# Optimization experiments

Hardware: AMD Instinct MI355X
Metric: run time of the kernel (lower is better)

Reference implementation:

```python
import jax, jax.numpy as jnp
import numpy as np

HEADS, HEAD_DIM, NQP, NVP = 12, 16, 4, 8
NODE_DIM, EDGE_DIM = 384, 128
B, N = 1, 768


def setup_inputs() -> dict:
    key = jax.random.key(0)
    ks = jax.random.split(key, 12)
    node_features = jax.random.normal(ks[0], (B, N, NODE_DIM), dtype=jnp.float32)
    edge_features = jax.random.normal(ks[1], (B, N, N, EDGE_DIM), dtype=jnp.float32)
    # random valid rotations via QR of gaussian matrices (well-conditioned for inverse)
    A = jax.random.normal(ks[2], (B, N, 3, 3), dtype=jnp.float32)
    Q, _ = jnp.linalg.qr(A)
    R = Q
    t = jax.random.normal(ks[3], (B, N, 3), dtype=jnp.float32)
    def lin(k, din, dout):
        return jax.random.normal(k, (din, dout), dtype=jnp.float32) / np.sqrt(din)
    Wqkv = lin(ks[4], NODE_DIM, 3 * HEADS * HEAD_DIM)
    Wvqk = lin(ks[5], NODE_DIM, 2 * 3 * NQP * HEADS)
    Wvv = lin(ks[6], NODE_DIM, 3 * NVP * HEADS)
    Webias = lin(ks[7], EDGE_DIM, HEADS)
    fin_in = HEADS * EDGE_DIM + HEADS * HEAD_DIM + HEADS * NVP * 4
    Wfin = lin(ks[8], fin_in, NODE_DIM)
    bfin = jnp.zeros((NODE_DIM,), dtype=jnp.float32)
    return {"node_features": node_features, "edge_features": edge_features,
            "R": R, "t": t, "Wqkv": Wqkv, "Wvqk": Wvqk, "Wvv": Wvv,
            "Webias": Webias, "Wfin": Wfin, "bfin": bfin}


def _ipa(node_features, edge_features, R, t, Wqkv, Wvqk, Wvv, Webias, Wfin, bfin):
    b, n, _ = node_features.shape
    h, d, p, pv = HEADS, HEAD_DIM, NQP, NVP
    # scalar q, k, v: [b, h, n, d]
    qkv = (node_features @ Wqkv).reshape(b, n, 3, h, d)
    sq, sk, sv = [jnp.transpose(qkv[:, :, i], (0, 2, 1, 3)) for i in range(3)]
    node_scalar = jnp.einsum('bhid,bhjd->bhij', sq, sk) * (d ** -0.5)
    edge_bias = jnp.einsum('bijd,dh->bhij', edge_features, Webias)
    # vector q/k in local frames: [b, h, n, p, 3]
    vqk = (node_features @ Wvqk).reshape(b, n, 2, h, p, 3)
    vq = jnp.transpose(vqk[:, :, 0], (0, 2, 1, 3, 4))
    vk = jnp.transpose(vqk[:, :, 1], (0, 2, 1, 3, 4))
    t_e = t[:, None, :, None, :]  # [b,1,n,1,3]
    gq = jnp.einsum('bnij,bhnpj->bhnpi', R, vq) + t_e
    gk = jnp.einsum('bnij,bhnpj->bhnpi', R, vk) + t_e
    # ||gk_i - gq_j||^2 summed over (p,3), expanded to avoid [b,h,n,n,p,3]
    wc = np.sqrt(2.0 / 9.0 / p) / 2.0
    k_sq = jnp.sum(gk * gk, axis=(-1, -2))  # [b,h,n]
    q_sq = jnp.sum(gq * gq, axis=(-1, -2))  # [b,h,n]
    cross = jnp.einsum('bhipd,bhjpd->bhij', gk, gq)
    dist = (k_sq[:, :, :, None] + q_sq[:, :, None, :] - 2.0 * cross) * wc
    attn = jax.nn.softmax((node_scalar + edge_bias - dist) * (3 ** -0.5), axis=-1)
    # aggregations
    edge_out = jnp.einsum('bhij,bijd->bihd', attn, edge_features)     # [b,n,h,edge_dim]
    scalar_out = jnp.einsum('bhij,bhjd->bihd', attn, sv)              # [b,n,h,d]
    vv = (node_features @ Wvv).reshape(b, n, h, pv, 3)
    vv = jnp.transpose(vv, (0, 2, 1, 3, 4))                            # [b,h,n,pv,3]
    gvv = jnp.einsum('bnij,bhnpj->bhnpi', R, vv) + t_e
    att_v = jnp.einsum('bhij,bhjpd->bihpd', attn, gvv)                # [b,n,h,pv,3]
    Rinv = jnp.linalg.inv(R)
    local_v = jnp.einsum('bnij,bnhpj->bnhpi', Rinv, att_v - t[:, :, None, None, :])
    v_len = jnp.sqrt(jnp.sum(local_v * local_v, axis=-1))             # [b,n,h,pv]
    combined = jnp.concatenate([
        edge_out.reshape(b, n, -1),
        scalar_out.reshape(b, n, -1),
        local_v.reshape(b, n, -1),
        v_len.reshape(b, n, -1),
    ], axis=-1)
    return node_features + combined @ Wfin + bfin


def reference(node_features, edge_features, R, t, Wqkv, Wvqk, Wvv, Webias, Wfin, bfin):
    return _ipa(node_features, edge_features, R, t, Wqkv, Wvqk, Wvv, Webias, Wfin, bfin)
```

## Files before the change

kernel.cpp:

```cpp
#include <hip/hip_runtime.h>
#include <cmath>


namespace {

constexpr int NN = 768;
constexpr int NH = 12;

constexpr float S3 = 0.5773502691896258f;
constexpr float C1 = 0.25f * S3;
constexpr float C2 = 0.23570226039551584f * S3;
constexpr float C3 = 0.11785113019775792f * S3;

typedef float f32x4 __attribute__((ext_vector_type(4)));
typedef short bf16x8 __attribute__((ext_vector_type(8)));
typedef unsigned int u32x4 __attribute__((ext_vector_type(4)));
typedef unsigned int u32x2 __attribute__((ext_vector_type(2)));
typedef _Float16 f16x2 __attribute__((ext_vector_type(2)));

#define LGKM0 asm volatile("s_waitcnt lgkmcnt(0)" ::: "memory")
#define SCHED0 __builtin_amdgcn_sched_barrier(0)

__device__ inline unsigned cvt_pk_bf16(float lo, float hi) {
  unsigned r;
  asm volatile("v_cvt_pk_bf16_f32 %0, %1, %2" : "=v"(r) : "v"(lo), "v"(hi));
  return r;
}

__device__ inline float fdot2(unsigned a, unsigned b, float c) {
#if __has_builtin(__builtin_amdgcn_fdot2)
  return __builtin_amdgcn_fdot2(__builtin_bit_cast(f16x2, a),
                                __builtin_bit_cast(f16x2, b), c, false);
#else
  union U { unsigned u; _Float16 h[2]; } x, y;
  x.u = a; y.u = b;
  return c + (float)x.h[0] * (float)y.h[0] + (float)x.h[1] * (float)y.h[1];
#endif
}

__device__ inline u32x2 tr_read(unsigned addr) {
  u32x2 d;
  asm volatile("ds_read_b64_tr_b16 %0, %1" : "=v"(d) : "v"(addr));
  return d;
}

__device__ inline f32x4 mfma16(u32x2 a, u32x2 b, f32x4 c) {
  asm volatile("v_mfma_f32_16x16x16_bf16 %0, %1, %2, %0"
               : "+v"(c) : "v"(a), "v"(b));
  return c;
}

__device__ inline unsigned pkf16(float a, float b) {
  union U { _Float16 h[2]; unsigned u; } x;
  x.h[0] = (_Float16)a; x.h[1] = (_Float16)b;
  return x.u;
}

__global__ __launch_bounds__(288) void k_proj(const float* __restrict__ node,
    const float* __restrict__ Wqkv, const float* __restrict__ Wvqk,
    const float* __restrict__ Wvv, float* __restrict__ proj) {
  __shared__ __align__(16) float nl[4][384];
  const int i0 = blockIdx.x * 4;
  const int tid = threadIdx.x;
  for (int idx = tid; idx < 4 * 384; idx += 288)
    ((float*)nl)[idx] = node[(size_t)i0 * 384 + idx];
  __syncthreads();
  const int c0 = tid * 4;
  const float* W; int ld, col;
  if (c0 < 576)      { W = Wqkv; ld = 576; col = c0; }
  else if (c0 < 864) { W = Wvqk; ld = 288; col = c0 - 576; }
  else               { W = Wvv;  ld = 288; col = c0 - 864; }
  float4 acc[4];
#pragma unroll
  for (int r = 0; r < 4; ++r) acc[r] = make_float4(0.f, 0.f, 0.f, 0.f);
#pragma unroll 4
  for (int k = 0; k < 384; ++k) {
    const float4 w4 = *(const float4*)&W[(size_t)k * ld + col];
#pragma unroll
    for (int r = 0; r < 4; ++r) {
      const float nv = nl[r][k];
      acc[r].x += nv * w4.x; acc[r].y += nv * w4.y;
      acc[r].z += nv * w4.z; acc[r].w += nv * w4.w;
    }
  }
#pragma unroll
  for (int r = 0; r < 4; ++r)
    *(float4*)&proj[(size_t)(i0 + r) * 1152 + c0] = acc[r];
}

__global__ __launch_bounds__(256) void k_geom(const float* __restrict__ proj,
    const float* __restrict__ R, const float* __restrict__ t,
    unsigned* __restrict__ Bph, unsigned* __restrict__ Sgh,
    float* __restrict__ V) {
  const int gid = blockIdx.x * 256 + threadIdx.x;
  if (gid >= NN * NH) return;
  const int n = gid / NH, h = gid % NH;
  const float* pr = proj + (size_t)n * 1152;
  const float* Rn = R + n * 9;
  const float t0 = t[n * 3 + 0], t1 = t[n * 3 + 1], t2 = t[n * 3 + 2];
  const size_t hn = (size_t)h * NN + n;
  unsigned* bp = Bph + hn * 16;
  unsigned* sg = Sgh + ((size_t)n * NH + h) * 16;
#pragma unroll
  for (int m = 0; m < 8; ++m) {
    bp[m] = pkf16(C1 * pr[(12 + h) * 16 + 2 * m], C1 * pr[(12 + h) * 16 + 2 * m + 1]);
    sg[m] = pkf16(pr[h * 16 + 2 * m], pr[h * 16 + 2 * m + 1]);
    V[hn * 40 + 2 * m]     = pr[(24 + h) * 16 + 2 * m];
    V[hn * 40 + 2 * m + 1] = pr[(24 + h) * 16 + 2 * m + 1];
  }
  float gq[12], gk[12];
  float qs = 0.f, ks = 0.f;
#pragma unroll
  for (int p = 0; p < 4; ++p) {
    {
      const float vx = pr[576 + (h * 4 + p) * 3 + 0];
      const float vy = pr[576 + (h * 4 + p) * 3 + 1];
      const float vz = pr[576 + (h * 4 + p) * 3 + 2];
      const float g0 = Rn[0] * vx + Rn[1] * vy + Rn[2] * vz + t0;
      const float g1 = Rn[3] * vx + Rn[4] * vy + Rn[5] * vz + t1;
      const float g2 = Rn[6] * vx + Rn[7] * vy + Rn[8] * vz + t2;
      gq[p * 3 + 0] = g0; gq[p * 3 + 1] = g1; gq[p * 3 + 2] = g2;
      qs += g0 * g0 + g1 * g1 + g2 * g2;
    }
    {
      const float vx = pr[576 + ((12 + h) * 4 + p) * 3 + 0];
      const float vy = pr[576 + ((12 + h) * 4 + p) * 3 + 1];
      const float vz = pr[576 + ((12 + h) * 4 + p) * 3 + 2];
      const float g0 = Rn[0] * vx + Rn[1] * vy + Rn[2] * vz + t0;
      const float g1 = Rn[3] * vx + Rn[4] * vy + Rn[5] * vz + t1;
      const float g2 = Rn[6] * vx + Rn[7] * vy + Rn[8] * vz + t2;
      gk[p * 3 + 0] = g0; gk[p * 3 + 1] = g1; gk[p * 3 + 2] = g2;
      ks += g0 * g0 + g1 * g1 + g2 * g2;
    }
  }
#pragma unroll
  for (int m = 0; m < 6; ++m) {
    bp[8 + m] = pkf16(C2 * gq[2 * m], C2 * gq[2 * m + 1]);
    sg[8 + m] = pkf16(gk[2 * m], gk[2 * m + 1]);
  }
  bp[14] = pkf16(-C3 * qs, 1.0f);
  sg[14] = pkf16(1.0f, -C3 * ks);
  bp[15] = 0u; sg[15] = 0u;
#pragma unroll
  for (int p = 0; p < 8; ++p) {
    const float vx = pr[864 + (h * 8 + p) * 3 + 0];
    const float vy = pr[864 + (h * 8 + p) * 3 + 1];
    const float vz = pr[864 + (h * 8 + p) * 3 + 2];
    V[hn * 40 + 16 + p * 3 + 0] = Rn[0] * vx + Rn[1] * vy + Rn[2] * vz + t0;
    V[hn * 40 + 16 + p * 3 + 1] = Rn[3] * vx + Rn[4] * vy + Rn[5] * vz + t1;
    V[hn * 40 + 16 + p * 3 + 2] = Rn[6] * vx + Rn[7] * vy + Rn[8] * vz + t2;
  }
}

__global__ __launch_bounds__(256, 3) void k_fused(
    const float* __restrict__ edge, const float* __restrict__ Webias,
    const unsigned* __restrict__ Bph, const unsigned* __restrict__ Sgh,
    unsigned* __restrict__ pTu, float* __restrict__ m_t,
    float* __restrict__ eout, float* __restrict__ msm,
    float* __restrict__ linv) {
  __shared__ __align__(16) unsigned short etS[4][2112];
  __shared__ __align__(16) float Osh[4][8][16][16];
  __shared__ float msh[4][16];
  __shared__ float lsh[4][16];
  const int i = blockIdx.x;
  const int tid = threadIdx.x;
  const int lane = tid & 63;
  const int w = __builtin_amdgcn_readfirstlane(tid >> 6);
  const int g = lane >> 4;
  const int c16 = lane & 15;
  const int hc = c16 < 12 ? c16 : 11;

  const unsigned etbase =
      (unsigned)(uintptr_t)(__attribute__((address_space(3))) unsigned short*)&etS[w][0];

  bf16x8 wbfrag[4];
#pragma unroll
  for (int kk = 0; kk < 4; ++kk) {
    union Pk { unsigned u[4]; bf16x8 v; } pk;
#pragma unroll
    for (int e2 = 0; e2 < 4; ++e2) {
      const int d = kk * 32 + g * 8 + 2 * e2;
      const float lo = (c16 < 12) ? S3 * Webias[d * 12 + c16] : 0.f;
      const float hi = (c16 < 12) ? S3 * Webias[(d + 1) * 12 + c16] : 0.f;
      pk.u[e2] = cvt_pk_bf16(lo, hi);
    }
    wbfrag[kk] = pk.v;
  }

  const unsigned* sgp = Sgh + ((size_t)i * NH + hc) * 16;
  const u32x4 sg0 = *(const u32x4*)(sgp + 0);
  const u32x4 sg1 = *(const u32x4*)(sgp + 4);
  const u32x4 sg2 = *(const u32x4*)(sgp + 8);
  const u32x4 sg3 = *(const u32x4*)(sgp + 12);

  float m = -3.0e38f;
  float lsum = 0.f;
  f32x4 acc[8];
#pragma unroll
  for (int dt = 0; dt < 8; ++dt) acc[dt] = (f32x4){0.f, 0.f, 0.f, 0.f};

  float4 ra[8];
  auto load8 = [&](int t) {
    const int jw = t * 64 + w * 16;
#pragma unroll
    for (int q = 0; q < 4; ++q) {
      const int f8 = lane + 64 * q;
      const int j = f8 >> 4, c8 = f8 & 15;
      const float* gp = &edge[((size_t)(i * NN + jw + j)) * 128 + c8 * 8];
      ra[2 * q]     = *(const float4*)gp;
      ra[2 * q + 1] = *(const float4*)(gp + 4);
    }
  };
  auto store8 = [&]() {
#pragma unroll
    for (int q = 0; q < 4; ++q) {
      const int f8 = lane + 64 * q;
      const int j = f8 >> 4, c8 = f8 & 15;
      u32x4 pk;
      pk.x = cvt_pk_bf16(ra[2 * q].x,     ra[2 * q].y);
      pk.y = cvt_pk_bf16(ra[2 * q].z,     ra[2 * q].w);
      pk.z = cvt_pk_bf16(ra[2 * q + 1].x, ra[2 * q + 1].y);
      pk.w = cvt_pk_bf16(ra[2 * q + 1].z, ra[2 * q + 1].w);
      *(u32x4*)&etS[w][(c8 >> 1) * 264 + j * 16 + 8 * (c8 & 1)] = pk;
    }
  };

  load8(0);

#pragma unroll 1
  for (int t = 0; t < 12; ++t) {
    const int tw = t * 4 + w;
    LGKM0;
    store8();
    SCHED0;
    if (t < 11) load8(t + 1);

    f32x4 ebacc = {0.f, 0.f, 0.f, 0.f};
#pragma unroll
    for (int kk = 0; kk < 4; ++kk) {
      const int dt = 2 * kk + (g >> 1);
      const bf16x8 a = *(const bf16x8*)&etS[w][dt * 264 + c16 * 16 + 8 * (g & 1)];
      ebacc = __builtin_amdgcn_mfma_f32_16x16x32_bf16(a, wbfrag[kk], ebacc, 0, 0, 0);
    }

    float lg[4];
#pragma unroll
    for (int r = 0; r < 4; ++r) {
      const unsigned* bpp = Bph + ((size_t)hc * NN + (tw * 16 + 4 * g + r)) * 16;
      const u32x4 b0 = *(const u32x4*)(bpp + 0);
      const u32x4 b1 = *(const u32x4*)(bpp + 4);
      const u32x4 b2 = *(const u32x4*)(bpp + 8);
      const u32x4 b3 = *(const u32x4*)(bpp + 12);
      float a = ebacc[r];
      a = fdot2(b0.x, sg0.x, a); a = fdot2(b0.y, sg0.y, a);
      a = fdot2(b0.z, sg0.z, a); a = fdot2(b0.w, sg0.w, a);
      a = fdot2(b1.x, sg1.x, a); a = fdot2(b1.y, sg1.y, a);
      a = fdot2(b1.z, sg1.z, a); a = fdot2(b1.w, sg1.w, a);
      a = fdot2(b2.x, sg2.x, a); a = fdot2(b2.y, sg2.y, a);
      a = fdot2(b2.z, sg2.z, a); a = fdot2(b2.w, sg2.w, a);
      a = fdot2(b3.x, sg3.x, a); a = fdot2(b3.y, sg3.y, a);
      a = fdot2(b3.z, sg3.z, a);
      lg[r] = a;
    }

    const float lmax = fmaxf(fmaxf(lg[0], lg[1]), fmaxf(lg[2], lg[3]));
    if (__any(lmax > m + 6.f)) {
      float tm = lmax;
      tm = fmaxf(tm, __shfl_xor(tm, 16, 64));
      tm = fmaxf(tm, __shfl_xor(tm, 32, 64));
      const float mn = fmaxf(m, tm);
      const float f = __expf(m - mn);
      m = mn;
      lsum *= f;
      float fr[4];
#pragma unroll
      for (int r = 0; r < 4; ++r) fr[r] = __shfl(f, 4 * g + r, 64);
#pragma unroll
      for (int dt = 0; dt < 8; ++dt) {
        acc[dt][0] *= fr[0]; acc[dt][1] *= fr[1];
        acc[dt][2] *= fr[2]; acc[dt][3] *= fr[3];
      }
    }
    float p0 = __expf(lg[0] - m), p1 = __expf(lg[1] - m);
    float p2 = __expf(lg[2] - m), p3 = __expf(lg[3] - m);
    lsum += (p0 + p1) + (p2 + p3);
    const unsigned pk0 = cvt_pk_bf16(p0, p1);
    const unsigned pk1 = cvt_pk_bf16(p2, p3);
    pTu[((size_t)i * 48 + tw) * 128 + g * 16 + c16]      = pk0;
    pTu[((size_t)i * 48 + tw) * 128 + 64 + g * 16 + c16] = pk1;
    if (g == 0) m_t[((size_t)i * 48 + tw) * 16 + c16] = m;

    u32x2 bfr[8];
#pragma unroll
    for (int dt = 0; dt < 8; ++dt) {
      const unsigned addr = etbase + (unsigned)(dt * 528 + g * 128 + c16 * 8);
      bfr[dt] = tr_read(addr);
    }
    LGKM0; SCHED0;
    u32x2 apk; apk.x = pk0; apk.y = pk1;
#pragma unroll
    for (int dt = 0; dt < 8; ++dt) acc[dt] = mfma16(apk, bfr[dt], acc[dt]);
  }

#pragma unroll
  for (int dt = 0; dt < 8; ++dt)
#pragma unroll
    for (int r = 0; r < 4; ++r)
      Osh[w][dt][c16][4 * g + r] = acc[dt][r];
  float ls = lsum;
  ls += __shfl_xor(ls, 16, 64);
  ls += __shfl_xor(ls, 32, 64);
  if (lane < 16) { msh[w][lane] = m; lsh[w][lane] = ls; }
  __syncthreads();
  for (int idx = tid; idx < 12 * 128; idx += 256) {
    const int h = idx >> 7, d = idx & 127;
    const int dt = d >> 4, dp = d & 15;
    const float m0 = msh[0][h], m1 = msh[1][h], m2 = msh[2][h], m3 = msh[3][h];
    const float mb = fmaxf(fmaxf(m0, m1), fmaxf(m2, m3));
    const float f0 = __expf(m0 - mb), f1 = __expf(m1 - mb);
    const float f2 = __expf(m2 - mb), f3 = __expf(m3 - mb);
    const float lb = lsh[0][h] * f0 + lsh[1][h] * f1 + lsh[2][h] * f2 + lsh[3][h] * f3;
    const float O = Osh[0][dt][dp][h] * f0 + Osh[1][dt][dp][h] * f1
                  + Osh[2][dt][dp][h] * f2 + Osh[3][dt][dp][h] * f3;
    eout[(size_t)i * 1536 + h * 128 + d] = O / lb;
    if (d == 0) {
      msm[(size_t)h * NN + i] = mb;
      linv[(size_t)h * NN + i] = 1.0f / lb;
    }
  }
}

__global__ __launch_bounds__(320) void k_scav(const unsigned* __restrict__ pTu,
    const float* __restrict__ m_t, const float* __restrict__ msm,
    const float* __restrict__ linv, const float* __restrict__ V,
    float* __restrict__ scav) {
  __shared__ __align__(16) float At[64][20];
  __shared__ __align__(16) float Vt[64][40];
  __shared__ __align__(16) float red[320 * 8];
  const int i0 = blockIdx.x * 16;
  const int h  = blockIdx.y;
  const int tid = threadIdx.x;
  const int js = tid / 80, rem = tid % 80;
  const int rg = rem / 20, cp = rem % 20;
  float2 a0 = {0.f, 0.f}, a1 = {0.f, 0.f}, a2 = {0.f, 0.f}, a3 = {0.f, 0.f};
  for (int jt = 0; jt < 12; ++jt) {
    __syncthreads();
    for (int idx = tid; idx < 1024; idx += 320) {
      const int r = idx >> 6, jj = idx & 63;
      const int i = i0 + r;
      const int tw = jt * 4 + (jj >> 4);
      const int gg = (jj & 15) >> 2, e = jj & 3;
      const unsigned u = pTu[((size_t)i * 48 + tw) * 128 + (e >> 1) * 64 + gg * 16 + h];
      const float p = __uint_as_float((e & 1) ? (u & 0xffff0000u) : (u << 16));
      const float fac = __expf(m_t[((size_t)i * 48 + tw) * 16 + h] - msm[(size_t)h * NN + i])
                      * linv[(size_t)h * NN + i];
      At[jj][r] = p * fac;
    }
    for (int idx = tid; idx < 2560; idx += 320) {
      const int jj = idx / 40, c = idx % 40;
      Vt[jj][c] = V[((size_t)h * NN + jt * 64 + jj) * 40 + c];
    }
    __syncthreads();
#pragma unroll 4
    for (int s = 0; s < 16; ++s) {
      const int jj = js * 16 + s;
      const float4 a4 = *(const float4*)&At[jj][rg * 4];
      const float2 b2 = *(const float2*)&Vt[jj][cp * 2];
      a0.x += a4.x * b2.x; a0.y += a4.x * b2.y;
      a1.x += a4.y * b2.x; a1.y += a4.y * b2.y;
      a2.x += a4.z * b2.x; a2.y += a4.z * b2.y;
      a3.x += a4.w * b2.x; a3.y += a4.w * b2.y;
    }
  }
  __syncthreads();
  *(float4*)&red[tid * 8 + 0] = make_float4(a0.x, a0.y, a1.x, a1.y);
  *(float4*)&red[tid * 8 + 4] = make_float4(a2.x, a2.y, a3.x, a3.y);
  __syncthreads();
  if (tid < 80) {
    const int rg2 = tid / 20, cp2 = tid % 20;
    float4 s0 = make_float4(0.f, 0.f, 0.f, 0.f), s1 = s0;
#pragma unroll
    for (int q = 0; q < 4; ++q) {
      const float4 r0 = *(const float4*)&red[(tid + q * 80) * 8 + 0];
      const float4 r1 = *(const float4*)&red[(tid + q * 80) * 8 + 4];
      s0.x += r0.x; s0.y += r0.y; s0.z += r0.z; s0.w += r0.w;
      s1.x += r1.x; s1.y += r1.y; s1.z += r1.z; s1.w += r1.w;
    }
    const size_t base = (size_t)h * NN + i0 + rg2 * 4;
    *(float2*)&scav[(base + 0) * 40 + cp2 * 2] = make_float2(s0.x, s0.y);
    *(float2*)&scav[(base + 1) * 40 + cp2 * 2] = make_float2(s0.z, s0.w);
    *(float2*)&scav[(base + 2) * 40 + cp2 * 2] = make_float2(s1.x, s1.y);
    *(float2*)&scav[(base + 3) * 40 + cp2 * 2] = make_float2(s1.z, s1.w);
  }
}

__global__ __launch_bounds__(256) void k_comb(
    const float* __restrict__ R, const float* __restrict__ t,
    const float* __restrict__ eout, const float* __restrict__ scav,
    float* __restrict__ comb) {
  const int i0 = blockIdx.x * 4;
  const int tid = threadIdx.x;
  __shared__ float rinv[4][9];
  __shared__ float tl[4][3];
  if (tid < 4) {
    const int i = i0 + tid;
    const float* Rn = R + i * 9;
    const float r00 = Rn[0], r01 = Rn[1], r02 = Rn[2];
    const float r10 = Rn[3], r11 = Rn[4], r12 = Rn[5];
    const float r20 = Rn[6], r21 = Rn[7], r22 = Rn[8];
    const float det = r00 * (r11 * r22 - r12 * r21)
                    - r01 * (r10 * r22 - r12 * r20)
                    + r02 * (r10 * r21 - r11 * r20);
    const float id = 1.0f / det;
    rinv[tid][0] = (r11 * r22 - r12 * r21) * id;
    rinv[tid][1] = (r02 * r21 - r01 * r22) * id;
    rinv[tid][2] = (r01 * r12 - r02 * r11) * id;
    rinv[tid][3] = (r12 * r20 - r10 * r22) * id;
    rinv[tid][4] = (r00 * r22 - r02 * r20) * id;
    rinv[tid][5] = (r02 * r10 - r00 * r12) * id;
    rinv[tid][6] = (r10 * r21 - r11 * r20) * id;
    rinv[tid][7] = (r01 * r20 - r00 * r21) * id;
    rinv[tid][8] = (r00 * r11 - r01 * r10) * id;
    tl[tid][0] = t[i * 3 + 0]; tl[tid][1] = t[i * 3 + 1]; tl[tid][2] = t[i * 3 + 2];
  }
  __syncthreads();
  for (int idx = tid; idx < 4 * 2112; idx += 256) {
    const int r = idx / 2112, k = idx % 2112;
    const int i = i0 + r;
    float val;
    if (k < 1536) {
      val = eout[(size_t)i * 1536 + k];
    } else if (k < 1728) {
      const int s = k - 1536, h = s >> 4, d = s & 15;
      val = scav[((size_t)h * NN + i) * 40 + d];
    } else if (k < 2016) {
      const int s = k - 1728, h = s / 24, rem = s % 24, p = rem / 3, x = rem % 3;
      const float* av = scav + ((size_t)h * NN + i) * 40 + 16 + p * 3;
      const float a0 = av[0] - tl[r][0], a1 = av[1] - tl[r][1], a2 = av[2] - tl[r][2];
      val = rinv[r][x * 3 + 0] * a0 + rinv[r][x * 3 + 1] * a1 + rinv[r][x * 3 + 2] * a2;
    } else {
      const int s = k - 2016, h = s >> 3, p = s & 7;
      const float* av = scav + ((size_t)h * NN + i) * 40 + 16 + p * 3;
      const float a0 = av[0] - tl[r][0], a1 = av[1] - tl[r][1], a2 = av[2] - tl[r][2];
      const float l0 = rinv[r][0] * a0 + rinv[r][1] * a1 + rinv[r][2] * a2;
      const float l1 = rinv[r][3] * a0 + rinv[r][4] * a1 + rinv[r][5] * a2;
      const float l2 = rinv[r][6] * a0 + rinv[r][7] * a1 + rinv[r][8] * a2;
      val = sqrtf(l0 * l0 + l1 * l1 + l2 * l2);
    }
    comb[(size_t)i * 2112 + k] = val;
  }
}

__global__ __launch_bounds__(256) void k_finalA(
    const float* __restrict__ comb, const float* __restrict__ Wfin,
    float* __restrict__ partial) {
  __shared__ __align__(16) float cl[64][36];
  __shared__ __align__(16) float wl[32][68];
  const int i0 = blockIdx.x * 64;
  const int c0 = blockIdx.y * 64;
  const int k0 = blockIdx.z * 192;
  const int tid = threadIdx.x;
  const int cq = tid & 15, rq = tid >> 4;
  float4 acc[4];
#pragma unroll
  for (int r = 0; r < 4; ++r) acc[r] = make_float4(0.f, 0.f, 0.f, 0.f);
  for (int sub = 0; sub < 6; ++sub) {
    const int kc = k0 + sub * 32;
    __syncthreads();
#pragma unroll
    for (int half = 0; half < 2; ++half) {
      const int qi = tid + half * 256;
      const int r = qi >> 3, kq = qi & 7;
      *(float4*)&cl[r][kq * 4] = *(const float4*)&comb[(size_t)(i0 + r) * 2112 + kc + kq * 4];
      const int kk = qi >> 4, cc = qi & 15;
      *(float4*)&wl[kk][cc * 4] = *(const float4*)&Wfin[(size_t)(kc + kk) * 384 + c0 + cc * 4];
    }
    __syncthreads();
#pragma unroll
    for (int k4 = 0; k4 < 8; ++k4) {
      float4 a[4], wv[4];
#pragma unroll
      for (int r = 0; r < 4; ++r) a[r] = *(const float4*)&cl[rq * 4 + r][k4 * 4];
#pragma unroll
      for (int q = 0; q < 4; ++q) wv[q] = *(const float4*)&wl[k4 * 4 + q][cq * 4];
#pragma unroll
      for (int r = 0; r < 4; ++r) {
        acc[r].x += a[r].x * wv[0].x + a[r].y * wv[1].x + a[r].z * wv[2].x + a[r].w * wv[3].x;
        acc[r].y += a[r].x * wv[0].y + a[r].y * wv[1].y + a[r].z * wv[2].y + a[r].w * wv[3].y;
        acc[r].z += a[r].x * wv[0].z + a[r].y * wv[1].z + a[r].z * wv[2].z + a[r].w * wv[3].z;
        acc[r].w += a[r].x * wv[0].w + a[r].y * wv[1].w + a[r].z * wv[2].w + a[r].w * wv[3].w;
      }
    }
  }
#pragma unroll
  for (int r = 0; r < 4; ++r)
    *(float4*)&partial[((size_t)blockIdx.z * NN + i0 + rq * 4 + r) * 384 + c0 + cq * 4] = acc[r];
}

__global__ __launch_bounds__(256) void k_finalB(const float* __restrict__ node,
    const float* __restrict__ partial, const float* __restrict__ bfin,
    float* __restrict__ out) {
  const int gid = blockIdx.x * 256 + threadIdx.x;
  const int i = gid / 96, cq = gid % 96;
  float4 v = *(const float4*)&node[(size_t)i * 384 + cq * 4];
  const float4 b = *(const float4*)&bfin[cq * 4];
  v.x += b.x; v.y += b.y; v.z += b.z; v.w += b.w;
#pragma unroll
  for (int s = 0; s < 11; ++s) {
    const float4 p = *(const float4*)&partial[((size_t)s * NN + i) * 384 + cq * 4];
    v.x += p.x; v.y += p.y; v.z += p.z; v.w += p.w;
  }
  *(float4*)&out[(size_t)i * 384 + cq * 4] = v;
}

}

extern "C" void kernel_launch(void* const* d_in, const int* in_sizes, int n_in,
                              void* d_out, int out_size, void* d_ws, size_t ws_size,
                              hipStream_t stream) {
  const float* node   = (const float*)d_in[0];
  const float* edge   = (const float*)d_in[1];
  const float* R      = (const float*)d_in[2];
  const float* t      = (const float*)d_in[3];
  const float* Wqkv   = (const float*)d_in[4];
  const float* Wvqk   = (const float*)d_in[5];
  const float* Wvv    = (const float*)d_in[6];
  const float* Webias = (const float*)d_in[7];
  const float* Wfin   = (const float*)d_in[8];
  const float* bfin   = (const float*)d_in[9];
  float* out = (float*)d_out;

  float* ws = (float*)d_ws;
  float*    proj = ws;
  float*    V    = proj + 884736;
  unsigned* Bph  = (unsigned*)(V + 368640);
  unsigned* Sgh  = Bph + 147456;
  unsigned* pTu  = Sgh + 147456;
  float*    m_t  = (float*)(pTu + 4718592);
  float*    eout = m_t + 589824;
  float*    scav = eout + 1179648;
  float*    msm  = scav + 368640;
  float*    linv = msm + 9216;
  float* comb    = (float*)pTu;
  float* partial = comb + 1622016;

  hipLaunchKernelGGL(k_proj, dim3(192), dim3(288), 0, stream,
                     node, Wqkv, Wvqk, Wvv, proj);
  hipLaunchKernelGGL(k_geom, dim3(36), dim3(256), 0, stream,
                     proj, R, t, Bph, Sgh, V);
  hipLaunchKernelGGL(k_fused, dim3(768), dim3(256), 0, stream,
                     edge, Webias, Bph, Sgh, pTu, m_t, eout, msm, linv);
  hipLaunchKernelGGL(k_scav, dim3(48, 12), dim3(320), 0, stream,
                     pTu, m_t, msm, linv, V, scav);
  hipLaunchKernelGGL(k_comb, dim3(192), dim3(256), 0, stream,
                     R, t, eout, scav, comb);
  hipLaunchKernelGGL(k_finalA, dim3(12, 6, 11), dim3(256), 0, stream,
                     comb, Wfin, partial);
  hipLaunchKernelGGL(k_finalB, dim3(288), dim3(256), 0, stream,
                     node, partial, bfin, out);
}
```

Measured before the change: 275.2 us.

## Double-buffer edge tile register loads and use coalesced contiguous float4 reads

Edge-feature tiles are now prefetched two iterations ahead into alternating register buffers, giving global loads more time to land before use. Each lane also reads consecutive float4s from a contiguous 16-row slab, making the loads fully coalesced, and the LDS store becomes 8-byte packed bf16 writes at transposed positions. This doubles the registers held for staging, which may reduce occupancy, and the narrower LDS stores may add bank conflicts.

Result: slower. 310.3 us (+12.7%).

```diff
diff --git a/kernel.cpp b/kernel.cpp
--- a/kernel.cpp
+++ b/kernel.cpp
@@ -199,41 +199,39 @@
 #pragma unroll
   for (int dt = 0; dt < 8; ++dt) acc[dt] = (f32x4){0.f, 0.f, 0.f, 0.f};
 
-  float4 ra[8];
-  auto load8 = [&](int t) {
-    const int jw = t * 64 + w * 16;
-#pragma unroll
-    for (int q = 0; q < 4; ++q) {
+  float4 rA[8], rB[8];
+  auto load8 = [&](int t, float4* r) {
+    const float* base = &edge[((size_t)(i * NN + t * 64 + w * 16)) * 128];
+#pragma unroll
+    for (int q = 0; q < 8; ++q) {
       const int f8 = lane + 64 * q;
-      const int j = f8 >> 4, c8 = f8 & 15;
-      const float* gp = &edge[((size_t)(i * NN + jw + j)) * 128 + c8 * 8];
-      ra[2 * q]     = *(const float4*)gp;
-      ra[2 * q + 1] = *(const float4*)(gp + 4);
+      r[q] = *(const float4*)&base[f8 * 4];
     }
   };
-  auto store8 = [&]() {
-#pragma unroll
-    for (int q = 0; q < 4; ++q) {
+  auto store8 = [&](const float4* r) {
+#pragma unroll
+    for (int q = 0; q < 8; ++q) {
       const int f8 = lane + 64 * q;
-      const int j = f8 >> 4, c8 = f8 & 15;
-      u32x4 pk;
-      pk.x = cvt_pk_bf16(ra[2 * q].x,     ra[2 * q].y);
-      pk.y = cvt_pk_bf16(ra[2 * q].z,     ra[2 * q].w);
-      pk.z = cvt_pk_bf16(ra[2 * q + 1].x, ra[2 * q + 1].y);
-      pk.w = cvt_pk_bf16(ra[2 * q + 1].z, ra[2 * q + 1].w);
-      *(u32x4*)&etS[w][(c8 >> 1) * 264 + j * 16 + 8 * (c8 & 1)] = pk;
+      const int j = f8 >> 5, db = f8 & 31;
+      u32x2 pk;
+      pk.x = cvt_pk_bf16(r[q].x, r[q].y);
+      pk.y = cvt_pk_bf16(r[q].z, r[q].w);
+      *(u32x2*)&etS[w][(db >> 2) * 264 + j * 16 + (db & 3) * 4] = pk;
     }
   };
 
-  load8(0);
+  load8(0, rA);
+  load8(1, rB);
 
 #pragma unroll 1
   for (int t = 0; t < 12; ++t) {
     const int tw = t * 4 + w;
     LGKM0;
-    store8();
+    if (t & 1) store8(rB); else store8(rA);
     SCHED0;
-    if (t < 11) load8(t + 1);
+    if (t + 2 < 12) {
+      if (t & 1) load8(t + 2, rB); else load8(t + 2, rA);
+    }
 
     f32x4 ebacc = {0.f, 0.f, 0.f, 0.f};
 #pragma unroll
```
